# Kernel optimization log

Hardware: AMD Instinct MI355X
Metric: run time of the kernel (lower is better)

## Reference

```python
import math
import jax, jax.numpy as jnp
import numpy as np
from jax import lax

UP = 2
DOWN = 2
M = 8
BETA = 2.5
FC = 0.5          # up_fc = down_fc = 0.5 (not 'critical' branch)
LRELU = 0.1

def _lpf_filter(factor):
    # Kaiser-windowed sinc, matches Resampler.__init__ (fc != 'critical' branch)
    Mf = M * factor
    n = np.arange(-Mf // 2, Mf // 2 + 1).astype(np.float32)   # 17 taps
    cutoff = FC * math.pi
    f = np.sin(cutoff * n) / (math.pi * n + 1e-8)
    f[len(n) // 2] = FC
    win = np.kaiser(Mf + 1, BETA).astype(np.float32)          # == torch.kaiser_window(.., periodic=False)
    return jnp.asarray(win * f, dtype=jnp.float32)

UP_FILT = _lpf_filter(UP)
DOWN_FILT = _lpf_filter(DOWN)

def _conv1d_same(x, w, groups=1):
    # x: (B, Cin, L), w: (Cout, Cin//groups, K) with odd K
    pad = (w.shape[-1] - 1) // 2
    return lax.conv_general_dilated(x, w, window_strides=(1,), padding=[(pad, pad)],
                                    dimension_numbers=('NCH', 'OIH', 'NCH'),
                                    feature_group_count=groups)

def _lpf(x, filt):
    # depthwise grouped FIR, padding='same'
    C = x.shape[1]
    f = jnp.broadcast_to(filt[None, None, :], (C, 1, filt.shape[0]))
    return _conv1d_same(x, f, groups=C)

def setup_inputs() -> dict:
    key = jax.random.key(0)
    ks = jax.random.split(key, 4)
    bs, c_in, c_out, w_dim, L, k = 16, 512, 512, 512, 2048, 3
    return {
        'x': jax.random.normal(ks[0], (bs, c_in, L), dtype=jnp.float32),
        'w': jax.random.normal(ks[1], (bs, w_dim), dtype=jnp.float32),
        'affine_w': jax.random.normal(ks[2], (c_in, w_dim), dtype=jnp.float32) * 0.02,
        'affine_b': jnp.ones((c_in,), dtype=jnp.float32),
        'conv_w': jax.random.normal(ks[3], (c_out, c_in, k), dtype=jnp.float32) * 0.05,
        'conv_b': jnp.zeros((c_out,), dtype=jnp.float32),
        'norm_ema': jnp.ones((), dtype=jnp.float32),
    }

def reference(x, w, affine_w, affine_b, conv_w, conv_b, norm_ema):
    # eval mode, equalized_lr=False, normalize=True
    x = x * lax.rsqrt(norm_ema)
    cond = w @ affine_w.T + affine_b                                      # (bs, c_in)
    # weight / style normalization
    Wn = conv_w * lax.rsqrt(jnp.mean(jnp.square(conv_w), axis=(1, 2), keepdims=True))
    s = cond * lax.rsqrt(jnp.mean(jnp.square(cond)))                      # (bs, c_in)
    # demod coeff: rsqrt(sum_{i,k} (Wn[o,i,k]*s[b,i])^2 + 1e-8)
    d = lax.rsqrt(jnp.einsum('oik,bi->bo', jnp.square(Wn), jnp.square(s)) + 1e-8)
    # modulate-conv-demodulate (equivalent to per-sample grouped conv with conv_w[None]*s*d)
    y = _conv1d_same(x * s[:, :, None], Wn) * d[:, :, None] + conv_b[None, :, None]
    # upsample: zero-insertion then interpolation LPF
    bs, C, L = y.shape
    y = jnp.pad(y[..., None], ((0, 0), (0, 0), (0, 0), (0, UP - 1))).reshape(bs, C, L * UP)
    y = _lpf(y, UP_FILT)
    # filtered nonlinearity
    y = jax.nn.leaky_relu(y, LRELU) * math.sqrt(2)
    # downsample: anti-alias LPF then decimate
    y = _lpf(y, DOWN_FILT)[:, :, ::DOWN]
    return y
```

## Files before the change

kernel.cpp:

```cpp
#include <hip/hip_runtime.h>
#include <cmath>

typedef __attribute__((ext_vector_type(8))) short short8;
typedef __attribute__((ext_vector_type(4))) float f32x4;

static __device__ __forceinline__ unsigned short f2bf(float x) {
  unsigned int u = __float_as_uint(x);
  unsigned int r = (u + 0x7FFFu + ((u >> 16) & 1u)) >> 16;
  return (unsigned short)r;
}
static __device__ __forceinline__ float bf2f(unsigned short u) {
  return __uint_as_float(((unsigned int)u) << 16);
}
static __device__ __forceinline__ void glds16(const unsigned short* g, unsigned short* l) {
  __builtin_amdgcn_global_load_lds((const __attribute__((address_space(1))) unsigned int*)(g),
                                   (__attribute__((address_space(3))) unsigned int*)(l), 16, 0, 0);
}

#define VWAIT(n) asm volatile("s_waitcnt vmcnt(" #n ")" ::: "memory")

__global__ __launch_bounds__(256) void k_pre1(const float* __restrict__ w,
    const float* __restrict__ aw, const float* __restrict__ ab,
    const float* __restrict__ cw, float* __restrict__ cond, float* __restrict__ ssum,
    float* __restrict__ W2, float* __restrict__ rinv, unsigned short* __restrict__ wpack) {
  __shared__ float red[4];
  int bid = blockIdx.x, t = threadIdx.x;
  if (bid < 128) {
    int outp = bid * 64 + (t >> 2);
    int sub = t & 3;
    int b = outp >> 9, i = outp & 511;
    const float4* wr = (const float4*)(w + b * 512);
    const float4* ar = (const float4*)(aw + i * 512);
    float acc = 0.f;
    #pragma unroll
    for (int jj = 0; jj < 32; ++jj) {
      int j = sub + jj * 4;
      float4 a = ar[j], v = wr[j];
      acc += a.x * v.x + a.y * v.y + a.z * v.z + a.w * v.w;
    }
    acc += __shfl_xor(acc, 1);
    acc += __shfl_xor(acc, 2);
    float s = 0.f;
    if (sub == 0) {
      float c = acc + ab[i];
      cond[outp] = c;
      s = c * c;
    }
    #pragma unroll
    for (int off = 4; off <= 32; off <<= 1) s += __shfl_xor(s, off);
    if ((t & 63) == 0) atomicAdd(ssum, s);
  } else {
    int o = bid - 128;
    const float* row = cw + o * 1536;
    float local = 0.f;
    for (int r = 0; r < 2; ++r) {
      int i = t + 256 * r;
      float a = row[3 * i], b = row[3 * i + 1], c = row[3 * i + 2];
      float w2 = a * a + b * b + c * c;
      W2[o * 512 + i] = w2;
      local += w2;
      int chunk = i >> 5;
      int laneo = (((i >> 3) & 3) << 4) + (o & 15);
      int e = i & 7;
      int base = (chunk * 32 + (o >> 4)) * 512 + laneo * 8 + e;
      wpack[base] = f2bf(a);
      wpack[base + 16 * 32 * 512] = f2bf(b);
      wpack[base + 2 * 16 * 32 * 512] = f2bf(c);
    }
    #pragma unroll
    for (int off = 32; off >= 1; off >>= 1) local += __shfl_down(local, off);
    if ((t & 63) == 0) red[t >> 6] = local;
    __syncthreads();
    if (t == 0) {
      float m = red[0] + red[1] + red[2] + red[3];
      rinv[o] = rsqrtf(m * (1.f / 1536.f));
    }
  }
}

__global__ __launch_bounds__(256) void k_pre2(const float* __restrict__ x,
    const float* __restrict__ W2, const float* __restrict__ cond,
    const float* __restrict__ rinv, const float* __restrict__ ssum,
    const float* __restrict__ nrm, float* __restrict__ coef,
    unsigned short* __restrict__ xsT) {
  __shared__ float shb[64 * 65];
  int bid = blockIdx.x, t = threadIdx.x;
  if (bid < 256) {
    int og = bid & 15, b = bid >> 4;
    int o = og * 32 + (t >> 3);
    int il = t & 7;
    float c0 = cond[b * 512 + t];
    float c1 = cond[b * 512 + t + 256];
    shb[t] = c0 * c0;
    shb[t + 256] = c1 * c1;
    __syncthreads();
    float acc = 0.f;
    #pragma unroll
    for (int jj = 0; jj < 16; ++jj) {
      int i = jj * 32 + il * 4;
      float4 wv = *(const float4*)(W2 + o * 512 + i);
      acc += wv.x * shb[i] + wv.y * shb[i + 1] + wv.z * shb[i + 2] + wv.w * shb[i + 3];
    }
    acc += __shfl_xor(acc, 1);
    acc += __shfl_xor(acc, 2);
    acc += __shfl_xor(acc, 4);
    if (il == 0) {
      float inv_ms = 8192.f / ssum[0];
      float ro = rinv[o];
      coef[b * 512 + o] = ro * rsqrtf(ro * ro * acc * inv_ms + 1e-8f);
    }
  } else {
    int xb = bid - 256;
    int lb = xb & 31, ib = (xb >> 5) & 7, b = xb >> 8;
    float (*tile)[65] = (float(*)[65])shb;
    int l0 = lb * 64, i0 = ib * 64;
    float sc = rsqrtf(ssum[0] * (1.f / 8192.f)) * rsqrtf(nrm[0]);
    int tr = t >> 4, tc = (t & 15) * 4;
    #pragma unroll
    for (int rr = 0; rr < 4; ++rr) {
      int il = rr * 16 + tr;
      float se = cond[b * 512 + i0 + il] * sc;
      float4 v = *(const float4*)(x + ((size_t)b * 512 + i0 + il) * 2048 + l0 + tc);
      tile[il][tc + 0] = v.x * se;
      tile[il][tc + 1] = v.y * se;
      tile[il][tc + 2] = v.z * se;
      tile[il][tc + 3] = v.w * se;
    }
    __syncthreads();
    int lr = t >> 3, ic = (t & 7) * 8;
    #pragma unroll
    for (int rr = 0; rr < 2; ++rr) {
      int ll = rr * 32 + lr;
      uint4 u;
      unsigned int pk[4];
      #pragma unroll
      for (int j = 0; j < 4; ++j) {
        unsigned short lo = f2bf(tile[ic + 2 * j][ll]);
        unsigned short hi = f2bf(tile[ic + 2 * j + 1][ll]);
        pk[j] = (unsigned int)lo | ((unsigned int)hi << 16);
      }
      u.x = pk[0]; u.y = pk[1]; u.z = pk[2]; u.w = pk[3];
      *(uint4*)(xsT + ((size_t)b * 2050 + 1 + l0 + ll) * 512 + i0 + ic) = u;
    }
    if (lb == 0 && t < 8) {
      uint4 z; z.x = 0; z.y = 0; z.z = 0; z.w = 0;
      *(uint4*)(xsT + ((size_t)b * 2050) * 512 + i0 + t * 8) = z;
    }
    if (lb == 31 && t < 8) {
      uint4 z; z.x = 0; z.y = 0; z.z = 0; z.w = 0;
      *(uint4*)(xsT + ((size_t)b * 2050 + 2049) * 512 + i0 + t * 8) = z;
    }
  }
}

#define STAGE_B(par, sub, c) { \
  _Pragma("unroll") for (int j_ = 0; j_ < 3; ++j_) { \
    int sb_ = wave * 130 + ((j_ < 2) ? j_ * 64 : 128); \
    int s_ = sb_ + ((j_ < 2) ? lane : (lane & 1)); \
    if (j_ < 2 || lane < 2) { \
      int col_ = ((s_ >> 3) << 1) | (((s_ >> 2) ^ (s_ >> 4)) & 1); \
      int q_ = ((s_ ^ (s_ >> 2) ^ (s_ >> 4)) & 1) | ((((s_ >> 1) ^ (s_ >> 3)) & 1) << 1); \
      const unsigned short* src_ = xsT + ((size_t)b * 2050 + l0 + col_) * 512 + (c) * 32 + q_ * 8; \
      glds16(src_, &Bl[par][sub][sb_ * 8]); \
    } \
  } }

#define LOAD_A(Ar, c) { \
  _Pragma("unroll") for (int k_ = 0; k_ < 3; ++k_) \
  _Pragma("unroll") for (int rg_ = 0; rg_ < 4; ++rg_) \
    Ar[k_ * 4 + rg_] = *(const short8*)(wpack + ((size_t)((k_ * 16 + (c)) * 32 + ob * 8 + wr * 4 + rg_)) * 512 + lane * 8); }

#define MFMA_STEP(Ar, par, sub) { \
  _Pragma("unroll") for (int k_ = 0; k_ < 3; ++k_) { \
    short8 bfr_[4]; \
    _Pragma("unroll") for (int cg_ = 0; cg_ < 4; ++cg_) { \
      int col_ = wc * 64 + cg_ * 16 + (lane & 15) + k_; \
      int byte_ = (col_ * 64 + ((lane >> 4) << 4)) ^ ((col_ & 7) << 4); \
      bfr_[cg_] = *(const short8*)((const char*)Bl[par][sub] + byte_); \
    } \
    _Pragma("unroll") for (int rg_ = 0; rg_ < 4; ++rg_) \
      _Pragma("unroll") for (int cg_ = 0; cg_ < 4; ++cg_) \
        acc[rg_][cg_] = __builtin_amdgcn_mfma_f32_16x16x32_bf16(Ar[k_ * 4 + rg_], bfr_[cg_], acc[rg_][cg_], 0, 0, 0); \
  } }

__global__ __launch_bounds__(256, 2) void k_main(const unsigned short* __restrict__ xsT,
    const unsigned short* __restrict__ wpack, const float* __restrict__ coef,
    const float* __restrict__ convb, unsigned short* __restrict__ y) {
  int lb = blockIdx.x, ob = blockIdx.y, b = blockIdx.z;
  int t = threadIdx.x, lane = t & 63, wave = t >> 6;
  int wr = wave >> 1, wc = wave & 1;
  int l0 = lb * 128, o0 = ob * 128;
  __shared__ __align__(16) unsigned short Bl[2][2][4160];
  f32x4 acc[4][4];
  f32x4 z4 = {0.f, 0.f, 0.f, 0.f};
  #pragma unroll
  for (int i = 0; i < 4; ++i)
    #pragma unroll
    for (int j = 0; j < 4; ++j) acc[i][j] = z4;

  short8 A[12];
  STAGE_B(0, 0, 0);
  STAGE_B(0, 1, 1);
  VWAIT(0);
  __builtin_amdgcn_s_barrier();

  #pragma unroll
  for (int p = 0; p < 8; ++p) {
    LOAD_A(A, 2 * p);
    if (p < 7) STAGE_B((p + 1) & 1, 0, 2 * p + 2);
    __builtin_amdgcn_sched_barrier(0);
    MFMA_STEP(A, p & 1, 0);
    __builtin_amdgcn_sched_barrier(0);
    LOAD_A(A, 2 * p + 1);
    if (p < 7) STAGE_B((p + 1) & 1, 1, 2 * p + 3);
    __builtin_amdgcn_sched_barrier(0);
    MFMA_STEP(A, p & 1, 1);
    __builtin_amdgcn_sched_barrier(0);
    VWAIT(0);
    __builtin_amdgcn_s_barrier();
  }

  int lq = lane >> 4, lrr = lane & 15;
  #pragma unroll
  for (int rg = 0; rg < 4; ++rg) {
    int o2 = o0 + wr * 64 + rg * 16 + lq * 4;
    float c0 = coef[b * 512 + o2 + 0], c1 = coef[b * 512 + o2 + 1];
    float c2 = coef[b * 512 + o2 + 2], c3 = coef[b * 512 + o2 + 3];
    float b0 = convb[o2 + 0], b1 = convb[o2 + 1];
    float b2 = convb[o2 + 2], b3 = convb[o2 + 3];
    #pragma unroll
    for (int cg = 0; cg < 4; ++cg) {
      int l = l0 + wc * 64 + cg * 16 + lrr;
      y[((size_t)b * 512 + o2 + 0) * 4096 + l] = f2bf(acc[rg][cg][0] * c0 + b0);
      y[((size_t)b * 512 + o2 + 1) * 4096 + l] = f2bf(acc[rg][cg][1] * c1 + b1);
      y[((size_t)b * 512 + o2 + 2) * 4096 + l] = f2bf(acc[rg][cg][2] * c2 + b2);
      y[((size_t)b * 512 + o2 + 3) * 4096 + l] = f2bf(acc[rg][cg][3] * c3 + b3);
    }
  }
}

struct Taps { float f[8]; };

__global__ __launch_bounds__(256) void k_filter(const unsigned short* __restrict__ ybuf,
    float* __restrict__ out, Taps tp) {
  int ch = blockIdx.x;
  int tir = threadIdx.x;
  int m0 = tir * 8;
  const unsigned short* yr = ybuf + (size_t)ch * 4096;
  uint4 z; z.x = 0u; z.y = 0u; z.z = 0u; z.w = 0u;
  uint4 v0, v1, v2;
  if (tir == 0) {
    v0 = z;
    v1 = *(const uint4*)(yr);
    v2 = *(const uint4*)(yr + 8);
  } else {
    const unsigned short* p = yr + m0 - 8;
    v0 = *(const uint4*)(p);
    v1 = *(const uint4*)(p + 8);
    v2 = *(const uint4*)(p + 16);
    if (tir == 255) v2 = z;
  }
  float f[24];
  {
    unsigned int wv[12] = {v0.x, v0.y, v0.z, v0.w, v1.x, v1.y, v1.z, v1.w,
                           v2.x, v2.y, v2.z, v2.w};
    #pragma unroll
    for (int s = 0; s < 12; ++s) {
      f[2 * s]     = bf2f((unsigned short)(wv[s] & 0xffffu));
      f[2 * s + 1] = bf2f((unsigned short)(wv[s] >> 16));
    }
  }
  const float s2 = 1.41421356237309515f;
  float ao[15];
  #pragma unroll
  for (int vv = 0; vv < 15; ++vv) {
    float u = 0.f;
    #pragma unroll
    for (int p = 0; p < 8; ++p) u += tp.f[p] * f[vv + p + 1];
    float a = (u >= 0.f ? u : 0.1f * u) * s2;
    ao[vv] = ((unsigned)(m0 - 4 + vv) < 2048u) ? a : 0.f;
  }
  const float ce = 0.35355339059327379f;
  float res[8];
  #pragma unroll
  for (int w = 0; w < 8; ++w) {
    float yv = f[w + 8];
    float s = ce * (yv >= 0.f ? yv : 0.1f * yv);
    #pragma unroll
    for (int q = 0; q < 8; ++q) s += tp.f[q] * ao[w + q];
    res[w] = s;
  }
  float4 o0; o0.x = res[0]; o0.y = res[1]; o0.z = res[2]; o0.w = res[3];
  float4 o1; o1.x = res[4]; o1.y = res[5]; o1.z = res[6]; o1.w = res[7];
  float* orow = out + (size_t)ch * 2048 + m0;
  *(float4*)orow = o0;
  *((float4*)orow + 1) = o1;
}

static double bessel_i0(double x) {
  double s = 1.0, term = 1.0;
  for (int m = 1; m < 30; ++m) {
    double h = x * 0.5 / (double)m;
    term *= h * h;
    s += term;
  }
  return s;
}

extern "C" void kernel_launch(void* const* d_in, const int* in_sizes, int n_in,
                              void* d_out, int out_size, void* d_ws, size_t ws_size,
                              hipStream_t stream) {
  (void)in_sizes; (void)n_in; (void)out_size; (void)ws_size;
  const float* x  = (const float*)d_in[0];
  const float* w  = (const float*)d_in[1];
  const float* aw = (const float*)d_in[2];
  const float* ab = (const float*)d_in[3];
  const float* cw = (const float*)d_in[4];
  const float* cb = (const float*)d_in[5];
  const float* ne = (const float*)d_in[6];
  float* out = (float*)d_out;
  char* ws = (char*)d_ws;

  float* ssum = (float*)(ws + 0);
  float* cond = (float*)(ws + 4096);
  float* coef = (float*)(ws + 36864);
  float* rinv = (float*)(ws + 69632);
  unsigned short* wpack = (unsigned short*)(ws + 73728);
  float* W2 = (float*)(ws + 3219456);
  unsigned short* xsT = (unsigned short*)(ws + 4268032);

  hipMemsetAsync(ssum, 0, 4, stream);
  k_pre1<<<640, 256, 0, stream>>>(w, aw, ab, cw, cond, ssum, W2, rinv, wpack);
  k_pre2<<<4352, 256, 0, stream>>>(x, W2, cond, rinv, ssum, ne, coef, xsT);
  k_main<<<dim3(16, 4, 16), 256, 0, stream>>>(xsT, wpack, coef, cb, (unsigned short*)d_out);

  Taps tp;
  {
    double beta = 2.5;
    double i0b = bessel_i0(beta);
    for (int p = 0; p < 8; ++p) {
      int j = 2 * p + 1;
      int n = j - 8;
      double f = sin(0.5 * M_PI * (double)n) / (M_PI * (double)n + 1e-8);
      double rr = (double)(j - 8) / 8.0;
      double win = bessel_i0(beta * sqrt(1.0 - rr * rr)) / i0b;
      tp.f[p] = (float)(win * f);
    }
  }
  k_filter<<<8192, 256, 0, stream>>>((const unsigned short*)d_out, out, tp);
}
```

Measured before the change: 208.1 us.

## Widen k_main tile to 256 columns with single-chunk double buffering and MFMA priority

The main modulated-conv GEMM kernel now computes 128x256 output tiles per block instead of 128x128, doubling accumulators per wave (4x8 fragments). Each A-fragment load from global memory is reused across twice as many MFMAs. The loop now stages one 32-channel chunk per iteration into a two-buffer LDS ring and raises wave priority around the MFMA block. The grid halves to 512 blocks, which risks lower occupancy and wave imbalance on the CUs, and the larger register footprint may cause spills under launch_bounds(256,2).

```diff
diff --git a/kernel.cpp b/kernel.cpp
--- a/kernel.cpp
+++ b/kernel.cpp
@@ -153,15 +153,16 @@
   }
 }
 
-#define STAGE_B(par, sub, c) { \
-  _Pragma("unroll") for (int j_ = 0; j_ < 3; ++j_) { \
-    int sb_ = wave * 130 + ((j_ < 2) ? j_ * 64 : 128); \
-    int s_ = sb_ + ((j_ < 2) ? lane : (lane & 1)); \
-    if (j_ < 2 || lane < 2) { \
-      int col_ = ((s_ >> 3) << 1) | (((s_ >> 2) ^ (s_ >> 4)) & 1); \
-      int q_ = ((s_ ^ (s_ >> 2) ^ (s_ >> 4)) & 1) | ((((s_ >> 1) ^ (s_ >> 3)) & 1) << 1); \
+#define STAGE_B(buf, c) { \
+  _Pragma("unroll") for (int j_ = 0; j_ < 5; ++j_) { \
+    int sb_ = wave * 258 + ((j_ < 4) ? j_ * 64 : 256); \
+    int s_ = sb_ + ((j_ < 4) ? lane : (lane & 1)); \
+    if (j_ < 4 || lane < 2) { \
+      int c0_ = ((s_ >> 2) ^ (s_ >> 4)) & 1; \
+      int col_ = ((s_ >> 3) << 1) | c0_; \
+      int q_ = ((s_ ^ c0_) & 1) | ((((s_ >> 1) ^ (s_ >> 3)) & 1) << 1); \
       const unsigned short* src_ = xsT + ((size_t)b * 2050 + l0 + col_) * 512 + (c) * 32 + q_ * 8; \
-      glds16(src_, &Bl[par][sub][sb_ * 8]); \
+      glds16(src_, &Bl[buf][sb_ * 8]); \
     } \
   } }
 
@@ -170,17 +171,22 @@
   _Pragma("unroll") for (int rg_ = 0; rg_ < 4; ++rg_) \
     Ar[k_ * 4 + rg_] = *(const short8*)(wpack + ((size_t)((k_ * 16 + (c)) * 32 + ob * 8 + wr * 4 + rg_)) * 512 + lane * 8); }
 
-#define MFMA_STEP(Ar, par, sub) { \
+#define MFMA_HALF(Ar, buf, k, cgb) { \
+  short8 bfr_[4]; \
+  _Pragma("unroll") for (int c2_ = 0; c2_ < 4; ++c2_) { \
+    int col_ = wc * 128 + ((cgb) + c2_) * 16 + (lane & 15) + (k); \
+    int byte_ = (col_ * 64 + ((lane >> 4) << 4)) ^ ((col_ & 7) << 4); \
+    bfr_[c2_] = *(const short8*)((const char*)Bl[buf] + byte_); \
+  } \
+  _Pragma("unroll") for (int rg_ = 0; rg_ < 4; ++rg_) \
+    _Pragma("unroll") for (int c2_ = 0; c2_ < 4; ++c2_) \
+      acc[rg_][(cgb) + c2_] = __builtin_amdgcn_mfma_f32_16x16x32_bf16(Ar[(k) * 4 + rg_], bfr_[c2_], acc[rg_][(cgb) + c2_], 0, 0, 0); \
+  }
+
+#define MFMA_CHUNK(Ar, buf) { \
   _Pragma("unroll") for (int k_ = 0; k_ < 3; ++k_) { \
-    short8 bfr_[4]; \
-    _Pragma("unroll") for (int cg_ = 0; cg_ < 4; ++cg_) { \
-      int col_ = wc * 64 + cg_ * 16 + (lane & 15) + k_; \
-      int byte_ = (col_ * 64 + ((lane >> 4) << 4)) ^ ((col_ & 7) << 4); \
-      bfr_[cg_] = *(const short8*)((const char*)Bl[par][sub] + byte_); \
-    } \
-    _Pragma("unroll") for (int rg_ = 0; rg_ < 4; ++rg_) \
-      _Pragma("unroll") for (int cg_ = 0; cg_ < 4; ++cg_) \
-        acc[rg_][cg_] = __builtin_amdgcn_mfma_f32_16x16x32_bf16(Ar[k_ * 4 + rg_], bfr_[cg_], acc[rg_][cg_], 0, 0, 0); \
+    MFMA_HALF(Ar, buf, k_, 0); \
+    MFMA_HALF(Ar, buf, k_, 4); \
   } }
 
 __global__ __launch_bounds__(256, 2) void k_main(const unsigned short* __restrict__ xsT,
@@ -189,32 +195,28 @@
   int lb = blockIdx.x, ob = blockIdx.y, b = blockIdx.z;
   int t = threadIdx.x, lane = t & 63, wave = t >> 6;
   int wr = wave >> 1, wc = wave & 1;
-  int l0 = lb * 128, o0 = ob * 128;
-  __shared__ __align__(16) unsigned short Bl[2][2][4160];
-  f32x4 acc[4][4];
+  int l0 = lb * 256, o0 = ob * 128;
+  __shared__ __align__(16) unsigned short Bl[2][8256];
+  f32x4 acc[4][8];
   f32x4 z4 = {0.f, 0.f, 0.f, 0.f};
   #pragma unroll
   for (int i = 0; i < 4; ++i)
     #pragma unroll
-    for (int j = 0; j < 4; ++j) acc[i][j] = z4;
+    for (int j = 0; j < 8; ++j) acc[i][j] = z4;
 
   short8 A[12];
-  STAGE_B(0, 0, 0);
-  STAGE_B(0, 1, 1);
+  STAGE_B(0, 0);
   VWAIT(0);
   __builtin_amdgcn_s_barrier();
 
-  #pragma unroll
-  for (int p = 0; p < 8; ++p) {
-    LOAD_A(A, 2 * p);
-    if (p < 7) STAGE_B((p + 1) & 1, 0, 2 * p + 2);
+  #pragma unroll 2
+  for (int c = 0; c < 16; ++c) {
+    LOAD_A(A, c);
+    if (c < 15) STAGE_B((c + 1) & 1, c + 1);
     __builtin_amdgcn_sched_barrier(0);
-    MFMA_STEP(A, p & 1, 0);
-    __builtin_amdgcn_sched_barrier(0);
-    LOAD_A(A, 2 * p + 1);
-    if (p < 7) STAGE_B((p + 1) & 1, 1, 2 * p + 3);
-    __builtin_amdgcn_sched_barrier(0);
-    MFMA_STEP(A, p & 1, 1);
+    __builtin_amdgcn_s_setprio(1);
+    MFMA_CHUNK(A, c & 1);
+    __builtin_amdgcn_s_setprio(0);
     __builtin_amdgcn_sched_barrier(0);
     VWAIT(0);
     __builtin_amdgcn_s_barrier();
@@ -229,8 +231,8 @@
     float b0 = convb[o2 + 0], b1 = convb[o2 + 1];
     float b2 = convb[o2 + 2], b3 = convb[o2 + 3];
     #pragma unroll
-    for (int cg = 0; cg < 4; ++cg) {
-      int l = l0 + wc * 64 + cg * 16 + lrr;
+    for (int cg = 0; cg < 8; ++cg) {
+      int l = l0 + wc * 128 + cg * 16 + lrr;
       y[((size_t)b * 512 + o2 + 0) * 4096 + l] = f2bf(acc[rg][cg][0] * c0 + b0);
       y[((size_t)b * 512 + o2 + 1) * 4096 + l] = f2bf(acc[rg][cg][1] * c1 + b1);
       y[((size_t)b * 512 + o2 + 2) * 4096 + l] = f2bf(acc[rg][cg][2] * c2 + b2);
@@ -332,7 +334,7 @@
   hipMemsetAsync(ssum, 0, 4, stream);
   k_pre1<<<640, 256, 0, stream>>>(w, aw, ab, cw, cond, ssum, W2, rinv, wpack);
   k_pre2<<<4352, 256, 0, stream>>>(x, W2, cond, rinv, ssum, ne, coef, xsT);
-  k_main<<<dim3(16, 4, 16), 256, 0, stream>>>(xsT, wpack, coef, cb, (unsigned short*)d_out);
+  k_main<<<dim3(8, 4, 16), 256, 0, stream>>>(xsT, wpack, coef, cb, (unsigned short*)d_out);
 
   Taps tp;
   {
```

New measurement: 196.5 us. 1.06x faster.
